# Kernel tuning notes

Hardware: AMD Instinct MI355X
Metric: run time of the kernel (lower is better)

Reference implementation:

```python
import jax, jax.numpy as jnp
import numpy as np

B, C, H, W = 512, 2048, 8, 8   # batch, backbone channels, feature-map HxW (cfg.output_hm_shape)
J = 30                          # smpl.pos_joint_num
CF = 512                        # conv output channels
EPS = 1e-5                      # BatchNorm eps


def setup_inputs() -> dict:
    key = jax.random.key(0)
    ks = jax.random.split(key, 10)
    D = J * (CF + 3)  # 15450
    return {
        "img_feat": jax.random.normal(ks[0], (B, C, H, W), jnp.float32),
        # joint coords in heatmap pixel space [0, W-1] (x, y, z)
        "joint_coord_img": jax.random.uniform(ks[1], (B, J, 3), jnp.float32) * (W - 1),
        "conv_w": jax.random.normal(ks[2], (CF, C), jnp.float32) * 0.02,
        "conv_b": jnp.zeros((CF,), jnp.float32),
        "bn_gamma": jnp.ones((CF,), jnp.float32),
        "bn_beta": jnp.zeros((CF,), jnp.float32),
        "bn_mean": jnp.zeros((CF,), jnp.float32),
        "bn_var": jnp.ones((CF,), jnp.float32),
        "root_w": jax.random.normal(ks[3], (6, D), jnp.float32) * 0.01,
        "root_b": jnp.zeros((6,), jnp.float32),
        "pose_w": jax.random.normal(ks[4], (126, D), jnp.float32) * 0.01,
        "pose_b": jnp.zeros((126,), jnp.float32),
        "shape_w": jax.random.normal(ks[5], (10, C), jnp.float32) * 0.01,
        "shape_b": jnp.zeros((10,), jnp.float32),
        "cam_w": jax.random.normal(ks[6], (3, C), jnp.float32) * 0.01,
        "cam_b": jnp.zeros((3,), jnp.float32),
    }


def _bilinear_sample(feat, xy):
    """Batched bilinear sample == F.grid_sample(align_corners=True, padding='zeros')
    with grid built directly from pixel coords in [0, W-1].
    feat: (B, Cf, H, W), xy: (B, J, 2) pixel coords -> (B, J, Cf)."""
    x, y = xy[..., 0], xy[..., 1]
    x0f, y0f = jnp.floor(x), jnp.floor(y)
    wx1, wy1 = x - x0f, y - y0f
    wx0, wy0 = 1.0 - wx1, 1.0 - wy1
    x0, y0 = x0f.astype(jnp.int32), y0f.astype(jnp.int32)
    x1, y1 = x0 + 1, y0 + 1

    def corner(yi, xi, wt):
        valid = (xi >= 0) & (xi < feat.shape[3]) & (yi >= 0) & (yi < feat.shape[2])
        yc = jnp.clip(yi, 0, feat.shape[2] - 1)
        xc = jnp.clip(xi, 0, feat.shape[3] - 1)
        # gather (B, Cf, J) via vmap over batch
        g = jax.vmap(lambda f, yy, xx: f[:, yy, xx])(feat, yc, xc)
        return g * (wt * valid.astype(feat.dtype))[:, None, :]

    out = (corner(y0, x0, wy0 * wx0) + corner(y0, x1, wy0 * wx1)
           + corner(y1, x0, wy1 * wx0) + corner(y1, x1, wy1 * wx1))
    return jnp.transpose(out, (0, 2, 1))  # (B, J, Cf)


def reference(img_feat, joint_coord_img, conv_w, conv_b, bn_gamma, bn_beta,
              bn_mean, bn_var, root_w, root_b, pose_w, pose_b,
              shape_w, shape_b, cam_w, cam_b):
    bsz = img_feat.shape[0]
    pooled = img_feat.mean(axis=(2, 3))                       # (B, 2048)
    shape_param = pooled @ shape_w.T + shape_b                # (B, 10)
    cam_param = pooled @ cam_w.T + cam_b                      # (B, 3)

    # 1x1 conv + BatchNorm (eval) + ReLU
    f = jnp.einsum('bchw,oc->bohw', img_feat, conv_w) + conv_b[None, :, None, None]
    f = (f - bn_mean[None, :, None, None]) * jax.lax.rsqrt(bn_var + EPS)[None, :, None, None]
    f = jax.nn.relu(f * bn_gamma[None, :, None, None] + bn_beta[None, :, None, None])

    # fused per-joint bilinear gather (replaces the per-joint python loop)
    img_feat_joints = _bilinear_sample(f, joint_coord_img[..., :2])  # (B, J, 512)
    feat = jnp.concatenate([img_feat_joints, joint_coord_img], axis=2)  # (B, J, 515)
    feat = feat.reshape(bsz, -1)                              # (B, 15450)

    root_pose = feat @ root_w.T + root_b                      # (B, 6)
    pose_param = feat @ pose_w.T + pose_b                     # (B, 126)
    return (root_pose, pose_param, shape_param, cam_param)
```

## Files before the change

kernel.cpp:

```cpp
#include <hip/hip_runtime.h>
#include <stdint.h>

typedef __attribute__((ext_vector_type(8))) short bf16x8;
typedef __attribute__((ext_vector_type(4))) float f32x4;

__device__ __forceinline__ unsigned short f2bf(float f) {
    union { float f; uint32_t u; } v; v.f = f;
    uint32_t r = (v.u + 0x7FFFu + ((v.u >> 16) & 1u)) >> 16;
    return (unsigned short)r;
}
__device__ __forceinline__ float bf2f(unsigned short u) {
    union { uint32_t u; float f; } v; v.u = ((uint32_t)u) << 16; return v.f;
}

#define WP_ELEMS  1081344
#define K2        15456
#define W2P_ELEMS (144 * K2)
#define B_OFF     42240

__global__ void pack_convw_kernel(const float* __restrict__ cw,
                                  const float* __restrict__ sw,
                                  const float* __restrict__ camw,
                                  unsigned short* __restrict__ Wp) {
    int gid = blockIdx.x * 256 + threadIdx.x;
    if (gid >= WP_ELEMS) return;
    int kt  = gid / 16896;
    int rem = gid - kt * 16896;
    int row = rem >> 5;
    int c   = rem & 31;
    int k   = kt * 32 + c;
    float v = 0.f;
    if (row < 512)      v = cw[row * 2048 + k];
    else if (row < 522) v = sw[(row - 512) * 2048 + k];
    else if (row < 525) v = camw[(row - 522) * 2048 + k];
    Wp[gid] = f2bf(v);
}

__global__ void pack_w2_kernel(const float* __restrict__ root_w,
                               const float* __restrict__ pose_w,
                               unsigned short* __restrict__ W2p) {
    int gid = blockIdx.x * 256 + threadIdx.x;
    if (gid >= W2P_ELEMS) return;
    int o2 = gid / K2;
    int kk = gid - o2 * K2;
    float v = 0.f;
    if (o2 < 132) {
        const float* wr = (o2 < 6) ? (root_w + o2 * 15450) : (pose_w + (o2 - 6) * 15450);
        if (kk < 15360) {
            int j = kk >> 9;
            int o = kk & 511;
            v = wr[j * 515 + o];
        } else {
            int c = kk - 15360;
            if (c < 90) {
                int j = c / 3, d = c - 3 * j;
                v = wr[j * 515 + 512 + d];
            }
        }
    }
    W2p[gid] = f2bf(v);
}

__global__ void bn_prep_kernel(const float* cb, const float* g, const float* be,
                               const float* m, const float* v, float* sbws) {
    int o = blockIdx.x * 256 + threadIdx.x;
    if (o >= 512) return;
    float s = g[o] * rsqrtf(v[o] + 1e-5f);
    sbws[2 * o]     = s;
    sbws[2 * o + 1] = be[o] + s * (cb[o] - m[o]);
}

__global__ __launch_bounds__(256, 2)
void conv_main_kernel(const float* __restrict__ img,
                      const float* __restrict__ jc,
                      const unsigned short* __restrict__ Wp,
                      const float* __restrict__ sbws,
                      const float* __restrict__ shape_b,
                      const float* __restrict__ cam_b,
                      unsigned short* __restrict__ sampled,
                      float* __restrict__ out) {
    __shared__ __align__(16) char smem[65536 + 256];
    const int t    = threadIdx.x;
    const int lane = t & 63;
    const int w    = t >> 6;
    const int l15  = lane & 15;
    const int quad = lane >> 4;
    const int b    = blockIdx.x;

    f32x4 acc[8][4];
    f32x4 accX;
    #pragma unroll
    for (int mi = 0; mi < 8; ++mi)
        #pragma unroll
        for (int nt = 0; nt < 4; ++nt)
            acc[mi][nt] = (f32x4){0.f, 0.f, 0.f, 0.f};
    accX = (f32x4){0.f, 0.f, 0.f, 0.f};

    const float* gBbase = img + (size_t)b * 131072 + (size_t)(w * 8) * 64 + lane;

    for (int kt = 0; kt < 64; ++kt) {
        __syncthreads();
        const int4* gA = (const int4*)(Wp + (size_t)kt * 16896);
        int4 ta[8];
        #pragma unroll
        for (int i = 0; i < 8; ++i) ta[i] = gA[t + 256 * i];
        int4 ta8;
        if (t < 64) ta8 = gA[t + 2048];
        const float* gB = gBbase + (size_t)(kt * 32) * 64;
        float fb[8];
        #pragma unroll
        for (int j = 0; j < 8; ++j) fb[j] = gB[j * 64];

        #pragma unroll
        for (int i = 0; i < 8; ++i) {
            int c2 = t + 256 * i;
            *(int4*)(smem + (c2 >> 2) * 80 + (c2 & 3) * 16) = ta[i];
        }
        if (t < 64) {
            int c2 = t + 2048;
            *(int4*)(smem + (c2 >> 2) * 80 + (c2 & 3) * 16) = ta8;
        }
        {
            int4 bv;
            bv.x = (int)((uint32_t)f2bf(fb[0]) | ((uint32_t)f2bf(fb[1]) << 16));
            bv.y = (int)((uint32_t)f2bf(fb[2]) | ((uint32_t)f2bf(fb[3]) << 16));
            bv.z = (int)((uint32_t)f2bf(fb[4]) | ((uint32_t)f2bf(fb[5]) << 16));
            bv.w = (int)((uint32_t)f2bf(fb[6]) | ((uint32_t)f2bf(fb[7]) << 16));
            *(int4*)(smem + B_OFF + lane * 80 + w * 16) = bv;
        }
        __syncthreads();

        bf16x8 bfr0 = *(const bf16x8*)(smem + B_OFF + (0  + l15) * 80 + quad * 16);
        bf16x8 bfr1 = *(const bf16x8*)(smem + B_OFF + (16 + l15) * 80 + quad * 16);
        bf16x8 bfr2 = *(const bf16x8*)(smem + B_OFF + (32 + l15) * 80 + quad * 16);
        bf16x8 bfr3 = *(const bf16x8*)(smem + B_OFF + (48 + l15) * 80 + quad * 16);
        #pragma unroll
        for (int mi = 0; mi < 8; ++mi) {
            bf16x8 afr = *(const bf16x8*)(smem + (w * 128 + mi * 16 + l15) * 80 + quad * 16);
            acc[mi][0] = __builtin_amdgcn_mfma_f32_16x16x32_bf16(afr, bfr0, acc[mi][0], 0, 0, 0);
            acc[mi][1] = __builtin_amdgcn_mfma_f32_16x16x32_bf16(afr, bfr1, acc[mi][1], 0, 0, 0);
            acc[mi][2] = __builtin_amdgcn_mfma_f32_16x16x32_bf16(afr, bfr2, acc[mi][2], 0, 0, 0);
            acc[mi][3] = __builtin_amdgcn_mfma_f32_16x16x32_bf16(afr, bfr3, acc[mi][3], 0, 0, 0);
        }
        {
            bf16x8 afrX = *(const bf16x8*)(smem + (512 + l15) * 80 + quad * 16);
            bf16x8 bfrW = *(const bf16x8*)(smem + B_OFF + (w * 16 + l15) * 80 + quad * 16);
            accX = __builtin_amdgcn_mfma_f32_16x16x32_bf16(afrX, bfrW, accX, 0, 0, 0);
        }
    }

    __syncthreads();
    const float2* sb2 = (const float2*)sbws;
    #pragma unroll
    for (int mi = 0; mi < 8; ++mi) {
        #pragma unroll
        for (int r = 0; r < 4; ++r) {
            int row = w * 128 + mi * 16 + quad * 4 + r;
            float2 sb = sb2[row];
            #pragma unroll
            for (int nt = 0; nt < 4; ++nt) {
                int col = nt * 16 + l15;
                float v = fmaxf(acc[mi][nt][r] * sb.x + sb.y, 0.f);
                *(unsigned short*)(smem + row * 128 + (((col + row) & 63) << 1)) = f2bf(v);
            }
        }
    }
    float* red = (float*)(smem + 65536);
    #pragma unroll
    for (int r = 0; r < 4; ++r) {
        float v = accX[r];
        v += __shfl_xor(v, 1);
        v += __shfl_xor(v, 2);
        v += __shfl_xor(v, 4);
        v += __shfl_xor(v, 8);
        if (l15 == 0) red[w * 16 + quad * 4 + r] = v;
    }
    __syncthreads();

    if (t < 16) {
        float v = (red[t] + red[16 + t] + red[32 + t] + red[48 + t]) * 0.015625f;
        if (t < 10)      out[67584 + b * 10 + t] = v + shape_b[t];
        else if (t < 13) out[72704 + b * 3 + (t - 10)] = v + cam_b[t - 10];
    }
    const float* jcb = jc + b * 90;
    if (t < 96) {
        float v = (t < 90) ? jcb[t] : 0.f;
        sampled[(size_t)b * K2 + 15360 + t] = f2bf(v);
    }

    unsigned int* outsamp = (unsigned int*)(sampled + (size_t)b * K2);
    const int o = 2 * t;
    for (int s = 0; s < 30; ++s) {
        float x = jcb[s * 3 + 0];
        float y = jcb[s * 3 + 1];
        float x0f = floorf(x), y0f = floorf(y);
        int x0 = (int)x0f, y0 = (int)y0f;
        int x1 = x0 + 1, y1 = y0 + 1;
        float wx1 = x - x0f, wy1 = y - y0f;
        float wx0 = 1.f - wx1, wy0 = 1.f - wy1;
        float vx0 = (x0 >= 0 && x0 < 8) ? 1.f : 0.f;
        float vx1 = (x1 >= 0 && x1 < 8) ? 1.f : 0.f;
        float vy0 = (y0 >= 0 && y0 < 8) ? 1.f : 0.f;
        float vy1 = (y1 >= 0 && y1 < 8) ? 1.f : 0.f;
        int cx0 = min(max(x0, 0), 7), cx1 = min(max(x1, 0), 7);
        int cy0 = min(max(y0, 0), 7), cy1 = min(max(y1, 0), 7);
        int p00 = cy0 * 8 + cx0, p01 = cy0 * 8 + cx1;
        int p10 = cy1 * 8 + cx0, p11 = cy1 * 8 + cx1;
        float w00 = wy0 * wx0 * vy0 * vx0, w01 = wy0 * wx1 * vy0 * vx1;
        float w10 = wy1 * wx0 * vy1 * vx0, w11 = wy1 * wx1 * vy1 * vx1;
        float vA = w00 * bf2f(*(unsigned short*)(smem + o * 128 + (((p00 + o) & 63) << 1)))
                 + w01 * bf2f(*(unsigned short*)(smem + o * 128 + (((p01 + o) & 63) << 1)))
                 + w10 * bf2f(*(unsigned short*)(smem + o * 128 + (((p10 + o) & 63) << 1)))
                 + w11 * bf2f(*(unsigned short*)(smem + o * 128 + (((p11 + o) & 63) << 1)));
        int o1 = o + 1;
        float vB = w00 * bf2f(*(unsigned short*)(smem + o1 * 128 + (((p00 + o1) & 63) << 1)))
                 + w01 * bf2f(*(unsigned short*)(smem + o1 * 128 + (((p01 + o1) & 63) << 1)))
                 + w10 * bf2f(*(unsigned short*)(smem + o1 * 128 + (((p10 + o1) & 63) << 1)))
                 + w11 * bf2f(*(unsigned short*)(smem + o1 * 128 + (((p11 + o1) & 63) << 1)));
        outsamp[s * 256 + t] = (uint32_t)f2bf(vA) | ((uint32_t)f2bf(vB) << 16);
    }
}

__global__ __launch_bounds__(256, 4)
void gemm2_kernel(const unsigned short* __restrict__ sampled,
                  const unsigned short* __restrict__ W2p,
                  float* __restrict__ part) {
    __shared__ __align__(16) char smem[16640];
    const int t    = threadIdx.x;
    const int lane = t & 63;
    const int w    = t >> 6;
    const int l15  = lane & 15;
    const int quad = lane >> 4;
    const int m0   = blockIdx.x * 64;
    const int j    = blockIdx.y;
    const int k0   = j * 512;
    const int ktn  = (j == 30) ? 3 : 16;

    f32x4 acc[9];
    #pragma unroll
    for (int nt = 0; nt < 9; ++nt) acc[nt] = (f32x4){0.f, 0.f, 0.f, 0.f};

    for (int kt = 0; kt < ktn; ++kt) {
        __syncthreads();
        {
            int r = t >> 2, ci = t & 3;
            int4 d = *(const int4*)(sampled + (size_t)(m0 + r) * K2 + k0 + kt * 32 + ci * 8);
            *(int4*)(smem + r * 80 + ci * 16) = d;
        }
        #pragma unroll
        for (int i = 0; i < 3; ++i) {
            int c2 = t + 256 * i;
            if (c2 < 576) {
                int r = c2 >> 2, ci = c2 & 3;
                int4 d = *(const int4*)(W2p + (size_t)r * K2 + k0 + kt * 32 + ci * 8);
                *(int4*)(smem + 5120 + r * 80 + ci * 16) = d;
            }
        }
        __syncthreads();
        bf16x8 a = *(const bf16x8*)(smem + (w * 16 + l15) * 80 + quad * 16);
        #pragma unroll
        for (int nt = 0; nt < 9; ++nt) {
            bf16x8 bfv = *(const bf16x8*)(smem + 5120 + (nt * 16 + l15) * 80 + quad * 16);
            acc[nt] = __builtin_amdgcn_mfma_f32_16x16x32_bf16(a, bfv, acc[nt], 0, 0, 0);
        }
    }
    float* pout = part + (size_t)(j * 8 + blockIdx.x) * 9216;
    #pragma unroll
    for (int nt = 0; nt < 9; ++nt) {
        #pragma unroll
        for (int r = 0; r < 4; ++r) {
            pout[(w * 16 + quad * 4 + r) * 144 + nt * 16 + l15] = acc[nt][r];
        }
    }
}

__global__ void reduce_out_kernel(const float* __restrict__ part,
                                  const float* __restrict__ root_b,
                                  const float* __restrict__ pose_b,
                                  float* __restrict__ out) {
    int gid = blockIdx.x * 256 + threadIdx.x;
    int m  = gid / 132;
    int o2 = gid - m * 132;
    float s = (o2 < 6) ? root_b[o2] : pose_b[o2 - 6];
    const float* p = part + (size_t)(m >> 6) * 9216 + (m & 63) * 144 + o2;
    #pragma unroll
    for (int j = 0; j < 31; ++j) s += p[(size_t)j * 8 * 9216];
    if (o2 < 6) out[m * 6 + o2] = s;
    else        out[3072 + m * 126 + (o2 - 6)] = s;
}

extern "C" void kernel_launch(void* const* d_in, const int* in_sizes, int n_in,
                              void* d_out, int out_size, void* d_ws, size_t ws_size,
                              hipStream_t stream) {
    const float* img     = (const float*)d_in[0];
    const float* jc      = (const float*)d_in[1];
    const float* conv_w  = (const float*)d_in[2];
    const float* conv_b  = (const float*)d_in[3];
    const float* bn_g    = (const float*)d_in[4];
    const float* bn_be   = (const float*)d_in[5];
    const float* bn_m    = (const float*)d_in[6];
    const float* bn_v    = (const float*)d_in[7];
    const float* root_w  = (const float*)d_in[8];
    const float* root_b  = (const float*)d_in[9];
    const float* pose_w  = (const float*)d_in[10];
    const float* pose_b  = (const float*)d_in[11];
    const float* shape_w = (const float*)d_in[12];
    const float* shape_b = (const float*)d_in[13];
    const float* cam_w   = (const float*)d_in[14];
    const float* cam_b   = (const float*)d_in[15];
    float* out = (float*)d_out;
    char* ws = (char*)d_ws;

    unsigned short* Wp   = (unsigned short*)(ws);
    unsigned short* W2p  = (unsigned short*)(ws + 2162688);
    unsigned short* samp = (unsigned short*)(ws + 6614016);
    float* part          = (float*)(ws + 22440960);
    float* sbws          = (float*)(ws + 31583232);

    pack_convw_kernel<<<4224, 256, 0, stream>>>(conv_w, shape_w, cam_w, Wp);
    pack_w2_kernel<<<8694, 256, 0, stream>>>(root_w, pose_w, W2p);
    bn_prep_kernel<<<2, 256, 0, stream>>>(conv_b, bn_g, bn_be, bn_m, bn_v, sbws);
    conv_main_kernel<<<512, 256, 0, stream>>>(img, jc, Wp, sbws, shape_b, cam_b,
                                              samp, out);
    gemm2_kernel<<<dim3(8, 31), 256, 0, stream>>>(samp, W2p, part);
    reduce_out_kernel<<<264, 256, 0, stream>>>(part, root_b, pose_b, out);
}
```

Measured before the change: 473.5 us.

## Process two batch items per conv block and prefetch next K-tile into registers

Result: slower. 587.6 us (+24.1%).

```diff
diff --git a/kernel.cpp b/kernel.cpp
--- a/kernel.cpp
+++ b/kernel.cpp
@@ -70,7 +70,7 @@
     sbws[2 * o + 1] = be[o] + s * (cb[o] - m[o]);
 }
 
-__global__ __launch_bounds__(256, 2)
+__global__ __launch_bounds__(512, 2)
 void conv_main_kernel(const float* __restrict__ img,
                       const float* __restrict__ jc,
                       const unsigned short* __restrict__ Wp,
@@ -79,13 +79,18 @@
                       const float* __restrict__ cam_b,
                       unsigned short* __restrict__ sampled,
                       float* __restrict__ out) {
-    __shared__ __align__(16) char smem[65536 + 256];
-    const int t    = threadIdx.x;
-    const int lane = t & 63;
-    const int w    = t >> 6;
-    const int l15  = lane & 15;
-    const int quad = lane >> 4;
-    const int b    = blockIdx.x;
+    __shared__ __align__(16) char smem[66048];
+    const int t     = threadIdx.x;
+    const int lane  = t & 63;
+    const int w     = t >> 6;
+    const int l15   = lane & 15;
+    const int quad  = lane >> 4;
+    const int bb    = t >> 8;
+    const int hw    = t & 63;
+    const int kch   = (t >> 6) & 3;
+    const int wbb   = w & 1;
+    const int wmh   = w >> 1;
+    const int b0    = blockIdx.x * 2;
 
     f32x4 acc[8][4];
     f32x4 accX;
@@ -96,29 +101,29 @@
             acc[mi][nt] = (f32x4){0.f, 0.f, 0.f, 0.f};
     accX = (f32x4){0.f, 0.f, 0.f, 0.f};
 
-    const float* gBbase = img + (size_t)b * 131072 + (size_t)(w * 8) * 64 + lane;
+    const float* gBbase = img + (size_t)(b0 + bb) * 131072 + (size_t)(kch * 8) * 64 + hw;
+
+    int4 ta[4], ta4;
+    float fb[8];
+    {
+        const int4* gA = (const int4*)Wp;
+        #pragma unroll
+        for (int i = 0; i < 4; ++i) ta[i] = gA[t + 512 * i];
+        if (t < 64) ta4 = gA[t + 2048];
+        #pragma unroll
+        for (int j = 0; j < 8; ++j) fb[j] = gBbase[j * 64];
+    }
 
     for (int kt = 0; kt < 64; ++kt) {
         __syncthreads();
-        const int4* gA = (const int4*)(Wp + (size_t)kt * 16896);
-        int4 ta[8];
-        #pragma unroll
-        for (int i = 0; i < 8; ++i) ta[i] = gA[t + 256 * i];
-        int4 ta8;
-        if (t < 64) ta8 = gA[t + 2048];
-        const float* gB = gBbase + (size_t)(kt * 32) * 64;
-        float fb[8];
-        #pragma unroll
-        for (int j = 0; j < 8; ++j) fb[j] = gB[j * 64];
-
-        #pragma unroll
-        for (int i = 0; i < 8; ++i) {
-            int c2 = t + 256 * i;
+        #pragma unroll
+        for (int i = 0; i < 4; ++i) {
+            int c2 = t + 512 * i;
             *(int4*)(smem + (c2 >> 2) * 80 + (c2 & 3) * 16) = ta[i];
         }
         if (t < 64) {
             int c2 = t + 2048;
-            *(int4*)(smem + (c2 >> 2) * 80 + (c2 & 3) * 16) = ta8;
+            *(int4*)(smem + (c2 >> 2) * 80 + (c2 & 3) * 16) = ta4;
         }
         {
             int4 bv;
@@ -126,17 +131,28 @@
             bv.y = (int)((uint32_t)f2bf(fb[2]) | ((uint32_t)f2bf(fb[3]) << 16));
             bv.z = (int)((uint32_t)f2bf(fb[4]) | ((uint32_t)f2bf(fb[5]) << 16));
             bv.w = (int)((uint32_t)f2bf(fb[6]) | ((uint32_t)f2bf(fb[7]) << 16));
-            *(int4*)(smem + B_OFF + lane * 80 + w * 16) = bv;
-        }
-        __syncthreads();
-
-        bf16x8 bfr0 = *(const bf16x8*)(smem + B_OFF + (0  + l15) * 80 + quad * 16);
-        bf16x8 bfr1 = *(const bf16x8*)(smem + B_OFF + (16 + l15) * 80 + quad * 16);
-        bf16x8 bfr2 = *(const bf16x8*)(smem + B_OFF + (32 + l15) * 80 + quad * 16);
-        bf16x8 bfr3 = *(const bf16x8*)(smem + B_OFF + (48 + l15) * 80 + quad * 16);
+            *(int4*)(smem + B_OFF + bb * 5120 + hw * 80 + kch * 16) = bv;
+        }
+        __syncthreads();
+
+        if (kt < 63) {
+            const int4* gA = (const int4*)(Wp + (size_t)(kt + 1) * 16896);
+            #pragma unroll
+            for (int i = 0; i < 4; ++i) ta[i] = gA[t + 512 * i];
+            if (t < 64) ta4 = gA[t + 2048];
+            const float* gB = gBbase + (size_t)((kt + 1) * 32) * 64;
+            #pragma unroll
+            for (int j = 0; j < 8; ++j) fb[j] = gB[j * 64];
+        }
+
+        const char* Bs = smem + B_OFF + wbb * 5120;
+        bf16x8 bfr0 = *(const bf16x8*)(Bs + (0  + l15) * 80 + quad * 16);
+        bf16x8 bfr1 = *(const bf16x8*)(Bs + (16 + l15) * 80 + quad * 16);
+        bf16x8 bfr2 = *(const bf16x8*)(Bs + (32 + l15) * 80 + quad * 16);
+        bf16x8 bfr3 = *(const bf16x8*)(Bs + (48 + l15) * 80 + quad * 16);
         #pragma unroll
         for (int mi = 0; mi < 8; ++mi) {
-            bf16x8 afr = *(const bf16x8*)(smem + (w * 128 + mi * 16 + l15) * 80 + quad * 16);
+            bf16x8 afr = *(const bf16x8*)(smem + (wmh * 128 + mi * 16 + l15) * 80 + quad * 16);
             acc[mi][0] = __builtin_amdgcn_mfma_f32_16x16x32_bf16(afr, bfr0, acc[mi][0], 0, 0, 0);
             acc[mi][1] = __builtin_amdgcn_mfma_f32_16x16x32_bf16(afr, bfr1, acc[mi][1], 0, 0, 0);
             acc[mi][2] = __builtin_amdgcn_mfma_f32_16x16x32_bf16(afr, bfr2, acc[mi][2], 0, 0, 0);
@@ -144,27 +160,12 @@
         }
         {
             bf16x8 afrX = *(const bf16x8*)(smem + (512 + l15) * 80 + quad * 16);
-            bf16x8 bfrW = *(const bf16x8*)(smem + B_OFF + (w * 16 + l15) * 80 + quad * 16);
-            accX = __builtin_amdgcn_mfma_f32_16x16x32_bf16(afrX, bfrW, accX, 0, 0, 0);
+            bf16x8 bfrX = *(const bf16x8*)(Bs + (wmh * 16 + l15) * 80 + quad * 16);
+            accX = __builtin_amdgcn_mfma_f32_16x16x32_bf16(afrX, bfrX, accX, 0, 0, 0);
         }
     }
 
     __syncthreads();
-    const float2* sb2 = (const float2*)sbws;
-    #pragma unroll
-    for (int mi = 0; mi < 8; ++mi) {
-        #pragma unroll
-        for (int r = 0; r < 4; ++r) {
-            int row = w * 128 + mi * 16 + quad * 4 + r;
-            float2 sb = sb2[row];
-            #pragma unroll
-            for (int nt = 0; nt < 4; ++nt) {
-                int col = nt * 16 + l15;
-                float v = fmaxf(acc[mi][nt][r] * sb.x + sb.y, 0.f);
-                *(unsigned short*)(smem + row * 128 + (((col + row) & 63) << 1)) = f2bf(v);
-            }
-        }
-    }
     float* red = (float*)(smem + 65536);
     #pragma unroll
     for (int r = 0; r < 4; ++r) {
@@ -175,49 +176,68 @@
         v += __shfl_xor(v, 8);
         if (l15 == 0) red[w * 16 + quad * 4 + r] = v;
     }
-    __syncthreads();
-
-    if (t < 16) {
-        float v = (red[t] + red[16 + t] + red[32 + t] + red[48 + t]) * 0.015625f;
-        if (t < 10)      out[67584 + b * 10 + t] = v + shape_b[t];
-        else if (t < 13) out[72704 + b * 3 + (t - 10)] = v + cam_b[t - 10];
-    }
-    const float* jcb = jc + b * 90;
-    if (t < 96) {
-        float v = (t < 90) ? jcb[t] : 0.f;
-        sampled[(size_t)b * K2 + 15360 + t] = f2bf(v);
-    }
-
-    unsigned int* outsamp = (unsigned int*)(sampled + (size_t)b * K2);
-    const int o = 2 * t;
-    for (int s = 0; s < 30; ++s) {
-        float x = jcb[s * 3 + 0];
-        float y = jcb[s * 3 + 1];
-        float x0f = floorf(x), y0f = floorf(y);
-        int x0 = (int)x0f, y0 = (int)y0f;
-        int x1 = x0 + 1, y1 = y0 + 1;
-        float wx1 = x - x0f, wy1 = y - y0f;
-        float wx0 = 1.f - wx1, wy0 = 1.f - wy1;
-        float vx0 = (x0 >= 0 && x0 < 8) ? 1.f : 0.f;
-        float vx1 = (x1 >= 0 && x1 < 8) ? 1.f : 0.f;
-        float vy0 = (y0 >= 0 && y0 < 8) ? 1.f : 0.f;
-        float vy1 = (y1 >= 0 && y1 < 8) ? 1.f : 0.f;
-        int cx0 = min(max(x0, 0), 7), cx1 = min(max(x1, 0), 7);
-        int cy0 = min(max(y0, 0), 7), cy1 = min(max(y1, 0), 7);
-        int p00 = cy0 * 8 + cx0, p01 = cy0 * 8 + cx1;
-        int p10 = cy1 * 8 + cx0, p11 = cy1 * 8 + cx1;
-        float w00 = wy0 * wx0 * vy0 * vx0, w01 = wy0 * wx1 * vy0 * vx1;
-        float w10 = wy1 * wx0 * vy1 * vx0, w11 = wy1 * wx1 * vy1 * vx1;
-        float vA = w00 * bf2f(*(unsigned short*)(smem + o * 128 + (((p00 + o) & 63) << 1)))
-                 + w01 * bf2f(*(unsigned short*)(smem + o * 128 + (((p01 + o) & 63) << 1)))
-                 + w10 * bf2f(*(unsigned short*)(smem + o * 128 + (((p10 + o) & 63) << 1)))
-                 + w11 * bf2f(*(unsigned short*)(smem + o * 128 + (((p11 + o) & 63) << 1)));
-        int o1 = o + 1;
-        float vB = w00 * bf2f(*(unsigned short*)(smem + o1 * 128 + (((p00 + o1) & 63) << 1)))
-                 + w01 * bf2f(*(unsigned short*)(smem + o1 * 128 + (((p01 + o1) & 63) << 1)))
-                 + w10 * bf2f(*(unsigned short*)(smem + o1 * 128 + (((p10 + o1) & 63) << 1)))
-                 + w11 * bf2f(*(unsigned short*)(smem + o1 * 128 + (((p11 + o1) & 63) << 1)));
-        outsamp[s * 256 + t] = (uint32_t)f2bf(vA) | ((uint32_t)f2bf(vB) << 16);
+
+    const float2* sb2 = (const float2*)sbws;
+    #pragma unroll
+    for (int p = 0; p < 2; ++p) {
+        if (p) __syncthreads();
+        if (wbb == p) {
+            #pragma unroll
+            for (int mi = 0; mi < 8; ++mi) {
+                #pragma unroll
+                for (int r = 0; r < 4; ++r) {
+                    int row = wmh * 128 + mi * 16 + quad * 4 + r;
+                    float2 sb = sb2[row];
+                    #pragma unroll
+                    for (int nt = 0; nt < 4; ++nt) {
+                        int col = nt * 16 + l15;
+                        float v = fmaxf(acc[mi][nt][r] * sb.x + sb.y, 0.f);
+                        *(unsigned short*)(smem + row * 128 + (((col + row) & 63) << 1)) = f2bf(v);
+                    }
+                }
+            }
+        }
+        __syncthreads();
+
+        const int b = b0 + p;
+        const float* jcb = jc + b * 90;
+        if (t < 16) {
+            float v = (red[(p    ) * 16 + t] + red[(p + 2) * 16 + t] +
+                       red[(p + 4) * 16 + t] + red[(p + 6) * 16 + t]) * 0.015625f;
+            if (t < 10)      out[67584 + b * 10 + t] = v + shape_b[t];
+            else if (t < 13) out[72704 + b * 3 + (t - 10)] = v + cam_b[t - 10];
+        }
+        if (t < 96) {
+            float v = (t < 90) ? jcb[t] : 0.f;
+            sampled[(size_t)b * K2 + 15360 + t] = f2bf(v);
+        }
+
+        unsigned short* outs = sampled + (size_t)b * K2;
+        const int o = t;
+        for (int s = 0; s < 30; ++s) {
+            float x = jcb[s * 3 + 0];
+            float y = jcb[s * 3 + 1];
+            float x0f = floorf(x), y0f = floorf(y);
+            int x0 = (int)x0f, y0 = (int)y0f;
+            int x1 = x0 + 1, y1 = y0 + 1;
+            float wx1 = x - x0f, wy1 = y - y0f;
+            float wx0 = 1.f - wx1, wy0 = 1.f - wy1;
+            float vx0 = (x0 >= 0 && x0 < 8) ? 1.f : 0.f;
+            float vx1 = (x1 >= 0 && x1 < 8) ? 1.f : 0.f;
+            float vy0 = (y0 >= 0 && y0 < 8) ? 1.f : 0.f;
+            float vy1 = (y1 >= 0 && y1 < 8) ? 1.f : 0.f;
+            int cx0 = min(max(x0, 0), 7), cx1 = min(max(x1, 0), 7);
+            int cy0 = min(max(y0, 0), 7), cy1 = min(max(y1, 0), 7);
+            int p00 = cy0 * 8 + cx0, p01 = cy0 * 8 + cx1;
+            int p10 = cy1 * 8 + cx0, p11 = cy1 * 8 + cx1;
+            float w00 = wy0 * wx0 * vy0 * vx0, w01 = wy0 * wx1 * vy0 * vx1;
+            float w10 = wy1 * wx0 * vy1 * vx0, w11 = wy1 * wx1 * vy1 * vx1;
+            float vA = w00 * bf2f(*(unsigned short*)(smem + o * 128 + (((p00 + o) & 63) << 1)))
+                     + w01 * bf2f(*(unsigned short*)(smem + o * 128 + (((p01 + o) & 63) << 1)))
+                     + w10 * bf2f(*(unsigned short*)(smem + o * 128 + (((p10 + o) & 63) << 1)))
+                     + w11 * bf2f(*(unsigned short*)(smem + o * 128 + (((p11 + o) & 63) << 1)));
+            outs[s * 512 + o] = f2bf(vA);
+        }
     }
 }
 
@@ -320,7 +340,7 @@
     pack_convw_kernel<<<4224, 256, 0, stream>>>(conv_w, shape_w, cam_w, Wp);
     pack_w2_kernel<<<8694, 256, 0, stream>>>(root_w, pose_w, W2p);
     bn_prep_kernel<<<2, 256, 0, stream>>>(conv_b, bn_g, bn_be, bn_m, bn_v, sbws);
-    conv_main_kernel<<<512, 256, 0, stream>>>(img, jc, Wp, sbws, shape_b, cam_b,
+    conv_main_kernel<<<256, 512, 0, stream>>>(img, jc, Wp, sbws, shape_b, cam_b,
                                               samp, out);
     gemm2_kernel<<<dim3(8, 31), 256, 0, stream>>>(samp, W2p, part);
     reduce_out_kernel<<<264, 256, 0, stream>>>(part, root_b, pose_b, out);
```

## Split conv GEMM across two blocks per batch and read weights directly from global

Applied to the files above, without the earlier changes.

Measured after the change: 513.9 us. +8.5%, slower.

```diff
diff --git a/kernel.cpp b/kernel.cpp
--- a/kernel.cpp
+++ b/kernel.cpp
@@ -16,7 +16,6 @@
 #define WP_ELEMS  1081344
 #define K2        15456
 #define W2P_ELEMS (144 * K2)
-#define B_OFF     42240
 
 __global__ void pack_convw_kernel(const float* __restrict__ cw,
                                   const float* __restrict__ sw,
@@ -70,7 +69,7 @@
     sbws[2 * o + 1] = be[o] + s * (cb[o] - m[o]);
 }
 
-__global__ __launch_bounds__(256, 2)
+__global__ __launch_bounds__(256, 4)
 void conv_main_kernel(const float* __restrict__ img,
                       const float* __restrict__ jc,
                       const unsigned short* __restrict__ Wp,
@@ -79,117 +78,122 @@
                       const float* __restrict__ cam_b,
                       unsigned short* __restrict__ sampled,
                       float* __restrict__ out) {
-    __shared__ __align__(16) char smem[65536 + 256];
+    __shared__ __align__(16) char smem[33280];
     const int t    = threadIdx.x;
     const int lane = t & 63;
     const int w    = t >> 6;
     const int l15  = lane & 15;
     const int quad = lane >> 4;
-    const int b    = blockIdx.x;
-
-    f32x4 acc[8][4];
-    f32x4 accX;
-    #pragma unroll
-    for (int mi = 0; mi < 8; ++mi)
+    const int b    = blockIdx.x >> 1;
+    const int mb   = blockIdx.x & 1;
+    const int R0   = mb << 8;
+
+    f32x4 acc[4][4];
+    f32x4 accX = (f32x4){0.f, 0.f, 0.f, 0.f};
+    #pragma unroll
+    for (int mi = 0; mi < 4; ++mi)
         #pragma unroll
         for (int nt = 0; nt < 4; ++nt)
             acc[mi][nt] = (f32x4){0.f, 0.f, 0.f, 0.f};
-    accX = (f32x4){0.f, 0.f, 0.f, 0.f};
-
-    const float* gBbase = img + (size_t)b * 131072 + (size_t)(w * 8) * 64 + lane;
+
+    const float* gB = img + (size_t)b * 131072 + w * 512 + lane;
+    int4 bv;
+    {
+        float fb[8];
+        #pragma unroll
+        for (int j = 0; j < 8; ++j) fb[j] = gB[j * 64];
+        bv.x = (int)((uint32_t)f2bf(fb[0]) | ((uint32_t)f2bf(fb[1]) << 16));
+        bv.y = (int)((uint32_t)f2bf(fb[2]) | ((uint32_t)f2bf(fb[3]) << 16));
+        bv.z = (int)((uint32_t)f2bf(fb[4]) | ((uint32_t)f2bf(fb[5]) << 16));
+        bv.w = (int)((uint32_t)f2bf(fb[6]) | ((uint32_t)f2bf(fb[7]) << 16));
+    }
 
     for (int kt = 0; kt < 64; ++kt) {
         __syncthreads();
-        const int4* gA = (const int4*)(Wp + (size_t)kt * 16896);
-        int4 ta[8];
-        #pragma unroll
-        for (int i = 0; i < 8; ++i) ta[i] = gA[t + 256 * i];
-        int4 ta8;
-        if (t < 64) ta8 = gA[t + 2048];
-        const float* gB = gBbase + (size_t)(kt * 32) * 64;
-        float fb[8];
-        #pragma unroll
-        for (int j = 0; j < 8; ++j) fb[j] = gB[j * 64];
-
-        #pragma unroll
-        for (int i = 0; i < 8; ++i) {
-            int c2 = t + 256 * i;
-            *(int4*)(smem + (c2 >> 2) * 80 + (c2 & 3) * 16) = ta[i];
-        }
-        if (t < 64) {
-            int c2 = t + 2048;
-            *(int4*)(smem + (c2 >> 2) * 80 + (c2 & 3) * 16) = ta8;
-        }
-        {
-            int4 bv;
+        *(int4*)(smem + lane * 80 + w * 16) = bv;
+        __syncthreads();
+
+        if (kt < 63) {
+            const float* g = gB + (size_t)(kt + 1) * 2048;
+            float fb[8];
+            #pragma unroll
+            for (int j = 0; j < 8; ++j) fb[j] = g[j * 64];
             bv.x = (int)((uint32_t)f2bf(fb[0]) | ((uint32_t)f2bf(fb[1]) << 16));
             bv.y = (int)((uint32_t)f2bf(fb[2]) | ((uint32_t)f2bf(fb[3]) << 16));
             bv.z = (int)((uint32_t)f2bf(fb[4]) | ((uint32_t)f2bf(fb[5]) << 16));
             bv.w = (int)((uint32_t)f2bf(fb[6]) | ((uint32_t)f2bf(fb[7]) << 16));
-            *(int4*)(smem + B_OFF + lane * 80 + w * 16) = bv;
-        }
-        __syncthreads();
-
-        bf16x8 bfr0 = *(const bf16x8*)(smem + B_OFF + (0  + l15) * 80 + quad * 16);
-        bf16x8 bfr1 = *(const bf16x8*)(smem + B_OFF + (16 + l15) * 80 + quad * 16);
-        bf16x8 bfr2 = *(const bf16x8*)(smem + B_OFF + (32 + l15) * 80 + quad * 16);
-        bf16x8 bfr3 = *(const bf16x8*)(smem + B_OFF + (48 + l15) * 80 + quad * 16);
-        #pragma unroll
-        for (int mi = 0; mi < 8; ++mi) {
-            bf16x8 afr = *(const bf16x8*)(smem + (w * 128 + mi * 16 + l15) * 80 + quad * 16);
-            acc[mi][0] = __builtin_amdgcn_mfma_f32_16x16x32_bf16(afr, bfr0, acc[mi][0], 0, 0, 0);
-            acc[mi][1] = __builtin_amdgcn_mfma_f32_16x16x32_bf16(afr, bfr1, acc[mi][1], 0, 0, 0);
-            acc[mi][2] = __builtin_amdgcn_mfma_f32_16x16x32_bf16(afr, bfr2, acc[mi][2], 0, 0, 0);
-            acc[mi][3] = __builtin_amdgcn_mfma_f32_16x16x32_bf16(afr, bfr3, acc[mi][3], 0, 0, 0);
-        }
-        {
-            bf16x8 afrX = *(const bf16x8*)(smem + (512 + l15) * 80 + quad * 16);
-            bf16x8 bfrW = *(const bf16x8*)(smem + B_OFF + (w * 16 + l15) * 80 + quad * 16);
-            accX = __builtin_amdgcn_mfma_f32_16x16x32_bf16(afrX, bfrW, accX, 0, 0, 0);
+        }
+
+        const unsigned short* WpK = Wp + (size_t)kt * 16896;
+        bf16x8 afr[4];
+        #pragma unroll
+        for (int mi = 0; mi < 4; ++mi)
+            afr[mi] = *(const bf16x8*)(WpK + (R0 + w * 64 + mi * 16 + l15) * 32 + quad * 8);
+
+        bf16x8 bfr0 = *(const bf16x8*)(smem + (0  + l15) * 80 + quad * 16);
+        bf16x8 bfr1 = *(const bf16x8*)(smem + (16 + l15) * 80 + quad * 16);
+        bf16x8 bfr2 = *(const bf16x8*)(smem + (32 + l15) * 80 + quad * 16);
+        bf16x8 bfr3 = *(const bf16x8*)(smem + (48 + l15) * 80 + quad * 16);
+
+        if (mb) {
+            bf16x8 afrX = *(const bf16x8*)(WpK + (512 + l15) * 32 + quad * 8);
+            bf16x8 bfrX = *(const bf16x8*)(smem + (w * 16 + l15) * 80 + quad * 16);
+            accX = __builtin_amdgcn_mfma_f32_16x16x32_bf16(afrX, bfrX, accX, 0, 0, 0);
+        }
+        #pragma unroll
+        for (int mi = 0; mi < 4; ++mi) {
+            acc[mi][0] = __builtin_amdgcn_mfma_f32_16x16x32_bf16(afr[mi], bfr0, acc[mi][0], 0, 0, 0);
+            acc[mi][1] = __builtin_amdgcn_mfma_f32_16x16x32_bf16(afr[mi], bfr1, acc[mi][1], 0, 0, 0);
+            acc[mi][2] = __builtin_amdgcn_mfma_f32_16x16x32_bf16(afr[mi], bfr2, acc[mi][2], 0, 0, 0);
+            acc[mi][3] = __builtin_amdgcn_mfma_f32_16x16x32_bf16(afr[mi], bfr3, acc[mi][3], 0, 0, 0);
         }
     }
 
     __syncthreads();
+    float* red = (float*)(smem + 32768);
+    if (mb) {
+        #pragma unroll
+        for (int r = 0; r < 4; ++r) {
+            float v = accX[r];
+            v += __shfl_xor(v, 1);
+            v += __shfl_xor(v, 2);
+            v += __shfl_xor(v, 4);
+            v += __shfl_xor(v, 8);
+            if (l15 == 0) red[w * 16 + quad * 4 + r] = v;
+        }
+    }
     const float2* sb2 = (const float2*)sbws;
     #pragma unroll
-    for (int mi = 0; mi < 8; ++mi) {
+    for (int mi = 0; mi < 4; ++mi) {
         #pragma unroll
         for (int r = 0; r < 4; ++r) {
-            int row = w * 128 + mi * 16 + quad * 4 + r;
-            float2 sb = sb2[row];
+            int lrow = w * 64 + mi * 16 + quad * 4 + r;
+            float2 sb = sb2[R0 + lrow];
             #pragma unroll
             for (int nt = 0; nt < 4; ++nt) {
                 int col = nt * 16 + l15;
                 float v = fmaxf(acc[mi][nt][r] * sb.x + sb.y, 0.f);
-                *(unsigned short*)(smem + row * 128 + (((col + row) & 63) << 1)) = f2bf(v);
+                *(unsigned short*)(smem + lrow * 128 + (((col + lrow) & 63) << 1)) = f2bf(v);
             }
         }
     }
-    float* red = (float*)(smem + 65536);
-    #pragma unroll
-    for (int r = 0; r < 4; ++r) {
-        float v = accX[r];
-        v += __shfl_xor(v, 1);
-        v += __shfl_xor(v, 2);
-        v += __shfl_xor(v, 4);
-        v += __shfl_xor(v, 8);
-        if (l15 == 0) red[w * 16 + quad * 4 + r] = v;
-    }
     __syncthreads();
 
-    if (t < 16) {
-        float v = (red[t] + red[16 + t] + red[32 + t] + red[48 + t]) * 0.015625f;
-        if (t < 10)      out[67584 + b * 10 + t] = v + shape_b[t];
-        else if (t < 13) out[72704 + b * 3 + (t - 10)] = v + cam_b[t - 10];
-    }
     const float* jcb = jc + b * 90;
-    if (t < 96) {
-        float v = (t < 90) ? jcb[t] : 0.f;
-        sampled[(size_t)b * K2 + 15360 + t] = f2bf(v);
-    }
-
-    unsigned int* outsamp = (unsigned int*)(sampled + (size_t)b * K2);
-    const int o = 2 * t;
+    if (mb) {
+        if (t < 16) {
+            float v = (red[t] + red[16 + t] + red[32 + t] + red[48 + t]) * 0.015625f;
+            if (t < 10)      out[67584 + b * 10 + t] = v + shape_b[t];
+            else if (t < 13) out[72704 + b * 3 + (t - 10)] = v + cam_b[t - 10];
+        }
+    } else {
+        if (t < 96) {
+            float v = (t < 90) ? jcb[t] : 0.f;
+            sampled[(size_t)b * K2 + 15360 + t] = f2bf(v);
+        }
+    }
+
+    unsigned short* outs = sampled + (size_t)b * K2 + R0;
     for (int s = 0; s < 30; ++s) {
         float x = jcb[s * 3 + 0];
         float y = jcb[s * 3 + 1];
@@ -208,16 +212,11 @@
         int p10 = cy1 * 8 + cx0, p11 = cy1 * 8 + cx1;
         float w00 = wy0 * wx0 * vy0 * vx0, w01 = wy0 * wx1 * vy0 * vx1;
         float w10 = wy1 * wx0 * vy1 * vx0, w11 = wy1 * wx1 * vy1 * vx1;
-        float vA = w00 * bf2f(*(unsigned short*)(smem + o * 128 + (((p00 + o) & 63) << 1)))
-                 + w01 * bf2f(*(unsigned short*)(smem + o * 128 + (((p01 + o) & 63) << 1)))
-                 + w10 * bf2f(*(unsigned short*)(smem + o * 128 + (((p10 + o) & 63) << 1)))
-                 + w11 * bf2f(*(unsigned short*)(smem + o * 128 + (((p11 + o) & 63) << 1)));
-        int o1 = o + 1;
-        float vB = w00 * bf2f(*(unsigned short*)(smem + o1 * 128 + (((p00 + o1) & 63) << 1)))
-                 + w01 * bf2f(*(unsigned short*)(smem + o1 * 128 + (((p01 + o1) & 63) << 1)))
-                 + w10 * bf2f(*(unsigned short*)(smem + o1 * 128 + (((p10 + o1) & 63) << 1)))
-                 + w11 * bf2f(*(unsigned short*)(smem + o1 * 128 + (((p11 + o1) & 63) << 1)));
-        outsamp[s * 256 + t] = (uint32_t)f2bf(vA) | ((uint32_t)f2bf(vB) << 16);
+        float vA = w00 * bf2f(*(unsigned short*)(smem + t * 128 + (((p00 + t) & 63) << 1)))
+                 + w01 * bf2f(*(unsigned short*)(smem + t * 128 + (((p01 + t) & 63) << 1)))
+                 + w10 * bf2f(*(unsigned short*)(smem + t * 128 + (((p10 + t) & 63) << 1)))
+                 + w11 * bf2f(*(unsigned short*)(smem + t * 128 + (((p11 + t) & 63) << 1)));
+        outs[s * 512 + t] = f2bf(vA);
     }
 }
 
@@ -320,8 +319,8 @@
     pack_convw_kernel<<<4224, 256, 0, stream>>>(conv_w, shape_w, cam_w, Wp);
     pack_w2_kernel<<<8694, 256, 0, stream>>>(root_w, pose_w, W2p);
     bn_prep_kernel<<<2, 256, 0, stream>>>(conv_b, bn_g, bn_be, bn_m, bn_v, sbws);
-    conv_main_kernel<<<512, 256, 0, stream>>>(img, jc, Wp, sbws, shape_b, cam_b,
-                                              samp, out);
+    conv_main_kernel<<<1024, 256, 0, stream>>>(img, jc, Wp, sbws, shape_b, cam_b,
+                                               samp, out);
     gemm2_kernel<<<dim3(8, 31), 256, 0, stream>>>(samp, W2p, part);
     reduce_out_kernel<<<264, 256, 0, stream>>>(part, root_b, pose_b, out);
 }
```
